# Optimization experiments

Hardware: AMD Instinct MI355X
Metric: run time of the kernel (lower is better)

Reference implementation:

```python
import jax, jax.numpy as jnp
import numpy as np

CUTOFF = 5.0       # module __init__ arg
BOX_L = 40.0       # side of cubic region positions are drawn from (OBC: no box passed)
N_ATOMS = 8192
MAX_PAIRS = 1_048_576  # static bound on directed pairs (expected ~550k)


def setup_inputs() -> dict:
    key = jax.random.key(0)
    positions = jax.random.uniform(key, (N_ATOMS, 3), dtype=jnp.float32) * BOX_L
    return {"positions": positions}


def _pairwise_dist(x):
    # Euclidean distance matrix via the gram trick (avoids [N,N,3] intermediate).
    sq = jnp.sum(x * x, axis=1)
    d2 = sq[:, None] + sq[None, :] - 2.0 * (x @ x.T)
    return jnp.sqrt(jnp.maximum(d2, 0.0))


def _safe_norm(dr):
    # norm with zero-safe gradient (padded pairs have dr == 0)
    d2 = jnp.sum(dr * dr, axis=1)
    ok = d2 > 0
    return jnp.where(ok, jnp.sqrt(jnp.where(ok, d2, 1.0)), 0.0)


def reference(positions):
    n = positions.shape[0]
    dist = _pairwise_dist(positions)                      # [N, N]
    mask = (dist < CUTOFF) & (~jnp.eye(n, dtype=bool))    # exclude self-pairs
    # torch.argwhere equivalent, padded to static size; padding -> (0, 0)
    i, j = jnp.nonzero(mask, size=MAX_PAIRS, fill_value=0)
    pairs = jnp.stack([i, j], axis=1).astype(jnp.int32)   # [MAX_PAIRS, 2]
    # pairs_buffer_scales: 1 where i < j else 0 (padding (0,0) -> 0)
    buffer_scales = (i < j).astype(jnp.int32)
    # pairs_ds (pbc_flag=False): ||r_j - r_i||
    dr = positions[j] - positions[i]                      # [MAX_PAIRS, 3]
    ds = _safe_norm(dr)
    return pairs, buffer_scales, ds
```

## Files before the change

### kernel.cpp

```cpp
#include <hip/hip_runtime.h>

#define MAXP 1048576
#define NATOMS 8192
#define D2_CUT 0x1.8ffffep+4f
#define CINV 0.175f
#define CAP 192

#define W_SORTPOS 0
#define W_SORTID  32768
#define W_ROWCNT  36864
#define W_GRPSUM  45056
#define W_CELLOFF 45568

__device__ __forceinline__ float sq3_nc(float x, float y, float z) {
#pragma clang fp contract(off)
  float a = x * x;
  float b = y * y;
  float c = z * z;
  return (a + b) + c;
}

__device__ __forceinline__ float d2_gram(float xi, float yi, float zi, float sqi,
                                         float xj, float yj, float zj, float sqj) {
#pragma clang fp contract(off)
  float g = xi * xj;
  g = __builtin_fmaf(yi, yj, g);
  g = __builtin_fmaf(zi, zj, g);
  float t = sqi + sqj;
  float d2 = t - 2.0f * g;
  return d2;
}

__device__ __forceinline__ float d2_direct(float xi, float yi, float zi,
                                           float xj, float yj, float zj) {
#pragma clang fp contract(off)
  float dx = xj - xi;
  float dy = yj - yi;
  float dz = zj - zi;
  float a = dx * dx;
  float b = dy * dy;
  float c = dz * dz;
  return (a + b) + c;
}

__device__ __forceinline__ int cellco(float v) {
  int c = (int)(v * CINV);
  return c < 0 ? 0 : (c > 6 ? 6 : c);
}

__global__ __launch_bounds__(1024) void nl_prep(const float* __restrict__ pos,
                                                float* __restrict__ out,
                                                float* __restrict__ ws) {
  const int tid = threadIdx.x;
  if (blockIdx.x != 0) {
    float4* o4 = (float4*)out;
    const int b = blockIdx.x - 1;
    for (int i = b * 1024 + tid; i < 1048576; i += 63 * 1024)
      o4[i] = make_float4(0.f, 0.f, 0.f, 0.f);
    if (blockIdx.x == 1 && tid < 512) ((int*)(ws + W_GRPSUM))[tid] = 0;
    return;
  }

  __shared__ int hcnt[343];
  __shared__ int hoff[344];
  __shared__ int hcur[343];
  __shared__ int s[512];
  if (tid < 343) { hcnt[tid] = 0; hcur[tid] = 0; }
  __syncthreads();

  float x[8], y[8], z[8];
  int cl[8];
#pragma unroll
  for (int k = 0; k < 8; ++k) {
    int a = tid + k * 1024;
    x[k] = pos[3 * a]; y[k] = pos[3 * a + 1]; z[k] = pos[3 * a + 2];
    cl[k] = cellco(x[k]) + 7 * cellco(y[k]) + 49 * cellco(z[k]);
    atomicAdd(&hcnt[cl[k]], 1);
  }
  __syncthreads();

  if (tid < 512) s[tid] = (tid < 343) ? hcnt[tid] : 0;
  __syncthreads();
  for (int off = 1; off < 512; off <<= 1) {
    int v = (tid < 512 && tid >= off) ? s[tid - off] : 0;
    __syncthreads();
    if (tid < 512) s[tid] += v;
    __syncthreads();
  }
  if (tid < 343) hoff[tid] = (tid == 0) ? 0 : s[tid - 1];
  if (tid == 343) hoff[343] = NATOMS;
  __syncthreads();
  if (tid < 344) ((int*)(ws + W_CELLOFF))[tid] = hoff[tid];

  unsigned short* sortid = (unsigned short*)(ws + W_SORTID);
  float4* sortpos = (float4*)(ws + W_SORTPOS);
#pragma unroll
  for (int k = 0; k < 8; ++k) {
    int slot = hoff[cl[k]] + atomicAdd(&hcur[cl[k]], 1);
    sortid[slot] = (unsigned short)(tid + k * 1024);
    sortpos[slot] = make_float4(x[k], y[k], z[k], sq3_nc(x[k], y[k], z[k]));
  }
}

__global__ __launch_bounds__(256, 8) void nl_count(float* __restrict__ ws) {
  const int lane = threadIdx.x & 63;
  const int wave = threadIdx.x >> 6;
  const int slot = blockIdx.x * 4 + wave;

  const float4* __restrict__ sp4 = (const float4*)(ws + W_SORTPOS);
  const unsigned short* __restrict__ sid = (const unsigned short*)(ws + W_SORTID);
  const int* __restrict__ celloff = (const int*)(ws + W_CELLOFF);
  int* rowcnt = (int*)(ws + W_ROWCNT);
  int* grpsum = (int*)(ws + W_GRPSUM);

  const float4 pi = sp4[slot];
  int cx = cellco(pi.x), cy = cellco(pi.y), cz = cellco(pi.z);
  int x0 = max(cx - 1, 0), x1 = min(cx + 1, 6);
  int y0 = max(cy - 1, 0), y1 = min(cy + 1, 6);
  int z0 = max(cz - 1, 0), z1 = min(cz + 1, 6);

  int cnt = 0;
  for (int icz = z0; icz <= z1; ++icz)
    for (int icy = y0; icy <= y1; ++icy) {
      int cb = 7 * icy + 49 * icz;
      int st = celloff[cb + x0];
      int en = celloff[cb + x1 + 1];
      for (int bb = st; bb < en; bb += 64) {
        int t = bb + lane;
        bool v = t < en;
        int t2 = v ? t : (en - 1);
        float4 p = sp4[t2];
        float d2 = d2_gram(pi.x, pi.y, pi.z, pi.w, p.x, p.y, p.z, p.w);
        cnt += (v && d2 < D2_CUT) ? 1 : 0;
      }
    }
  for (int off = 32; off > 0; off >>= 1) cnt += __shfl_down(cnt, off, 64);
  if (lane == 0) {
    const int rid = sid[slot];
    rowcnt[rid] = cnt - 1;
    atomicAdd(&grpsum[rid >> 6], cnt - 1);
  }
}

__global__ __launch_bounds__(256, 8) void nl_write(const float* __restrict__ pos,
                                                   float* __restrict__ out,
                                                   const float* __restrict__ ws) {
  __shared__ unsigned int bmap[4][256];
  __shared__ unsigned short stj[4][CAP];
  const int lane = threadIdx.x & 63;
  const int wave = threadIdx.x >> 6;
  const int slot = blockIdx.x * 4 + wave;

  const float4* __restrict__ sp4 = (const float4*)(ws + W_SORTPOS);
  const unsigned short* __restrict__ sid = (const unsigned short*)(ws + W_SORTID);
  const int* __restrict__ celloff = (const int*)(ws + W_CELLOFF);
  const int* __restrict__ rowcnt = (const int*)(ws + W_ROWCNT);
  const int* __restrict__ grpsum = (const int*)(ws + W_GRPSUM);

#pragma unroll
  for (int q = 0; q < 4; ++q) bmap[wave][lane + 64 * q] = 0u;

  const float4 pi = sp4[slot];
  const int rid = sid[slot];

  const int G = rid >> 6;
  int pre = ((lane < G) ? grpsum[lane] : 0) +
            ((lane + 64 < G) ? grpsum[lane + 64] : 0) +
            ((lane < (rid & 63)) ? rowcnt[(rid & ~63) + lane] : 0);
  for (int off = 32; off > 0; off >>= 1) pre += __shfl_down(pre, off, 64);
  const int ro = __shfl(pre, 0, 64);

  int cx = cellco(pi.x), cy = cellco(pi.y), cz = cellco(pi.z);
  int x0 = max(cx - 1, 0), x1 = min(cx + 1, 6);
  int y0 = max(cy - 1, 0), y1 = min(cy + 1, 6);
  int z0 = max(cz - 1, 0), z1 = min(cz + 1, 6);

  for (int icz = z0; icz <= z1; ++icz)
    for (int icy = y0; icy <= y1; ++icy) {
      int cb = 7 * icy + 49 * icz;
      int st = celloff[cb + x0];
      int en = celloff[cb + x1 + 1];
      for (int bb = st; bb < en; bb += 64) {
        int t = bb + lane;
        bool v = t < en;
        int t2 = v ? t : (en - 1);
        float4 p = sp4[t2];
        int jd = sid[t2];
        float d2 = d2_gram(pi.x, pi.y, pi.z, pi.w, p.x, p.y, p.z, p.w);
        if (v && d2 < D2_CUT)
          atomicOr(&bmap[wave][jd >> 5], 1u << (jd & 31));
      }
    }
  if (lane == 0)
    atomicAnd(&bmap[wave][rid >> 5], ~(1u << (rid & 31)));

  int ktot = 0;
#pragma unroll
  for (int seg = 0; seg < 4; ++seg) {
    int w = seg * 64 + lane;
    unsigned bits = bmap[wave][w];
    int pc = __popc(bits);
    int incl = pc;
    for (int d = 1; d < 64; d <<= 1) {
      int u = __shfl_up(incl, d, 64);
      if (lane >= d) incl += u;
    }
    int bpos = ktot + incl - pc;
    while (bits) {
      int b = __builtin_ctz(bits);
      bits &= bits - 1;
      if (bpos < CAP) stj[wave][bpos] = (unsigned short)(w * 32 + b);
      ++bpos;
    }
    ktot += __shfl(incl, 63, 64);
  }

  int k = ktot > CAP ? CAP : ktot;
  for (int s2 = lane; s2 < k; s2 += 64) {
    int j = stj[wave][s2];
    int o = ro + s2;
    if ((unsigned)o < MAXP) {
      float xj = pos[3 * j], yj = pos[3 * j + 1], zj = pos[3 * j + 2];
      float ds = sqrtf(d2_direct(pi.x, pi.y, pi.z, xj, yj, zj));
      ((float2*)out)[o] = make_float2((float)rid, (float)j);
      out[2 * MAXP + o] = (rid < j) ? 1.0f : 0.0f;
      out[3 * MAXP + o] = ds;
    }
  }
}

extern "C" void kernel_launch(void* const* d_in, const int* in_sizes, int n_in,
                              void* d_out, int out_size, void* d_ws, size_t ws_size,
                              hipStream_t stream) {
  const float* pos = (const float*)d_in[0];
  float* out = (float*)d_out;
  float* ws = (float*)d_ws;

  nl_prep<<<64, 1024, 0, stream>>>(pos, out, ws);
  nl_count<<<2048, 256, 0, stream>>>(ws);
  nl_write<<<2048, 256, 0, stream>>>(pos, out, ws);
}
```

Baseline: 105.2 us.

## Merge neighbor count and bitmap pass, buffer neighbor lists for emit

Replaces the separate count pass and the rescan in the write pass with a single detect kernel. It builds each row's neighbor bitmap once, writes the compacted j list to a workspace buffer, and records per-row counts and group sums. A new emit kernel then computes the offsets and writes the outputs from the buffered j lists, so the cell-neighborhood distance scan runs once instead of twice. Output zeroing moves to its own kernel ahead of the single-block prep kernel. The cost is an extra launch plus workspace traffic for the j buffer (8192 rows by CAP ushorts).

```diff
diff --git a/kernel.cpp b/kernel.cpp
--- a/kernel.cpp
+++ b/kernel.cpp
@@ -11,6 +11,7 @@
 #define W_ROWCNT  36864
 #define W_GRPSUM  45056
 #define W_CELLOFF 45568
+#define W_JBUF    46080
 
 __device__ __forceinline__ float sq3_nc(float x, float y, float z) {
 #pragma clang fp contract(off)
@@ -48,23 +49,23 @@
   return c < 0 ? 0 : (c > 6 ? 6 : c);
 }
 
+__global__ __launch_bounds__(256) void nl_pack(float* __restrict__ out,
+                                               float* __restrict__ ws) {
+  const int gtid = blockIdx.x * 256 + threadIdx.x;
+  float4* o4 = (float4*)out;
+#pragma unroll
+  for (int k = 0; k < 16; ++k)
+    o4[k * 65536 + gtid] = make_float4(0.f, 0.f, 0.f, 0.f);
+  if (gtid < 512) ((int*)(ws + W_GRPSUM))[gtid] = 0;
+}
+
 __global__ __launch_bounds__(1024) void nl_prep(const float* __restrict__ pos,
-                                                float* __restrict__ out,
                                                 float* __restrict__ ws) {
-  const int tid = threadIdx.x;
-  if (blockIdx.x != 0) {
-    float4* o4 = (float4*)out;
-    const int b = blockIdx.x - 1;
-    for (int i = b * 1024 + tid; i < 1048576; i += 63 * 1024)
-      o4[i] = make_float4(0.f, 0.f, 0.f, 0.f);
-    if (blockIdx.x == 1 && tid < 512) ((int*)(ws + W_GRPSUM))[tid] = 0;
-    return;
-  }
-
   __shared__ int hcnt[343];
   __shared__ int hoff[344];
   __shared__ int hcur[343];
   __shared__ int s[512];
+  const int tid = threadIdx.x;
   if (tid < 343) { hcnt[tid] = 0; hcur[tid] = 0; }
   __syncthreads();
 
@@ -102,7 +103,9 @@
   }
 }
 
-__global__ __launch_bounds__(256, 8) void nl_count(float* __restrict__ ws) {
+__global__ __launch_bounds__(256, 8) void nl_detect(float* __restrict__ ws) {
+  __shared__ unsigned int bmap[4][256];
+  __shared__ unsigned short stj[4][CAP];
   const int lane = threadIdx.x & 63;
   const int wave = threadIdx.x >> 6;
   const int slot = blockIdx.x * 4 + wave;
@@ -112,64 +115,13 @@
   const int* __restrict__ celloff = (const int*)(ws + W_CELLOFF);
   int* rowcnt = (int*)(ws + W_ROWCNT);
   int* grpsum = (int*)(ws + W_GRPSUM);
-
-  const float4 pi = sp4[slot];
-  int cx = cellco(pi.x), cy = cellco(pi.y), cz = cellco(pi.z);
-  int x0 = max(cx - 1, 0), x1 = min(cx + 1, 6);
-  int y0 = max(cy - 1, 0), y1 = min(cy + 1, 6);
-  int z0 = max(cz - 1, 0), z1 = min(cz + 1, 6);
-
-  int cnt = 0;
-  for (int icz = z0; icz <= z1; ++icz)
-    for (int icy = y0; icy <= y1; ++icy) {
-      int cb = 7 * icy + 49 * icz;
-      int st = celloff[cb + x0];
-      int en = celloff[cb + x1 + 1];
-      for (int bb = st; bb < en; bb += 64) {
-        int t = bb + lane;
-        bool v = t < en;
-        int t2 = v ? t : (en - 1);
-        float4 p = sp4[t2];
-        float d2 = d2_gram(pi.x, pi.y, pi.z, pi.w, p.x, p.y, p.z, p.w);
-        cnt += (v && d2 < D2_CUT) ? 1 : 0;
-      }
-    }
-  for (int off = 32; off > 0; off >>= 1) cnt += __shfl_down(cnt, off, 64);
-  if (lane == 0) {
-    const int rid = sid[slot];
-    rowcnt[rid] = cnt - 1;
-    atomicAdd(&grpsum[rid >> 6], cnt - 1);
-  }
-}
-
-__global__ __launch_bounds__(256, 8) void nl_write(const float* __restrict__ pos,
-                                                   float* __restrict__ out,
-                                                   const float* __restrict__ ws) {
-  __shared__ unsigned int bmap[4][256];
-  __shared__ unsigned short stj[4][CAP];
-  const int lane = threadIdx.x & 63;
-  const int wave = threadIdx.x >> 6;
-  const int slot = blockIdx.x * 4 + wave;
-
-  const float4* __restrict__ sp4 = (const float4*)(ws + W_SORTPOS);
-  const unsigned short* __restrict__ sid = (const unsigned short*)(ws + W_SORTID);
-  const int* __restrict__ celloff = (const int*)(ws + W_CELLOFF);
-  const int* __restrict__ rowcnt = (const int*)(ws + W_ROWCNT);
-  const int* __restrict__ grpsum = (const int*)(ws + W_GRPSUM);
+  unsigned short* jbuf = (unsigned short*)(ws + W_JBUF);
 
 #pragma unroll
   for (int q = 0; q < 4; ++q) bmap[wave][lane + 64 * q] = 0u;
 
   const float4 pi = sp4[slot];
   const int rid = sid[slot];
-
-  const int G = rid >> 6;
-  int pre = ((lane < G) ? grpsum[lane] : 0) +
-            ((lane + 64 < G) ? grpsum[lane + 64] : 0) +
-            ((lane < (rid & 63)) ? rowcnt[(rid & ~63) + lane] : 0);
-  for (int off = 32; off > 0; off >>= 1) pre += __shfl_down(pre, off, 64);
-  const int ro = __shfl(pre, 0, 64);
-
   int cx = cellco(pi.x), cy = cellco(pi.y), cz = cellco(pi.z);
   int x0 = max(cx - 1, 0), x1 = min(cx + 1, 6);
   int y0 = max(cy - 1, 0), y1 = min(cy + 1, 6);
@@ -216,8 +168,41 @@
   }
 
   int k = ktot > CAP ? CAP : ktot;
+  for (int s2 = lane; s2 < k; s2 += 64)
+    jbuf[slot * CAP + s2] = stj[wave][s2];
+  if (lane == 0) {
+    rowcnt[rid] = ktot;
+    atomicAdd(&grpsum[rid >> 6], ktot);
+  }
+}
+
+__global__ __launch_bounds__(256, 8) void nl_emit(const float* __restrict__ pos,
+                                                  float* __restrict__ out,
+                                                  const float* __restrict__ ws) {
+  const int lane = threadIdx.x & 63;
+  const int wave = threadIdx.x >> 6;
+  const int slot = blockIdx.x * 4 + wave;
+
+  const float4* __restrict__ sp4 = (const float4*)(ws + W_SORTPOS);
+  const unsigned short* __restrict__ sid = (const unsigned short*)(ws + W_SORTID);
+  const int* __restrict__ rowcnt = (const int*)(ws + W_ROWCNT);
+  const int* __restrict__ grpsum = (const int*)(ws + W_GRPSUM);
+  const unsigned short* __restrict__ jbuf = (const unsigned short*)(ws + W_JBUF);
+
+  const float4 pi = sp4[slot];
+  const int rid = sid[slot];
+
+  const int G = rid >> 6;
+  int pre = ((lane < G) ? grpsum[lane] : 0) +
+            ((lane + 64 < G) ? grpsum[lane + 64] : 0) +
+            ((lane < (rid & 63)) ? rowcnt[(rid & ~63) + lane] : 0);
+  for (int off = 32; off > 0; off >>= 1) pre += __shfl_down(pre, off, 64);
+  const int ro = __shfl(pre, 0, 64);
+
+  int k = rowcnt[rid];
+  if (k > CAP) k = CAP;
   for (int s2 = lane; s2 < k; s2 += 64) {
-    int j = stj[wave][s2];
+    int j = jbuf[slot * CAP + s2];
     int o = ro + s2;
     if ((unsigned)o < MAXP) {
       float xj = pos[3 * j], yj = pos[3 * j + 1], zj = pos[3 * j + 2];
@@ -236,7 +221,8 @@
   float* out = (float*)d_out;
   float* ws = (float*)d_ws;
 
-  nl_prep<<<64, 1024, 0, stream>>>(pos, out, ws);
-  nl_count<<<2048, 256, 0, stream>>>(ws);
-  nl_write<<<2048, 256, 0, stream>>>(pos, out, ws);
-}
+  nl_pack<<<256, 256, 0, stream>>>(out, ws);
+  nl_prep<<<1, 1024, 0, stream>>>(pos, ws);
+  nl_detect<<<2048, 256, 0, stream>>>(ws);
+  nl_emit<<<2048, 256, 0, stream>>>(pos, out, ws);
+}
```

New measurement: 104.1 us. No clear change (-1.0%).
